# Performance work log

Hardware: AMD Instinct MI355X
Metric: run time of the kernel (lower is better)

The kernel has to match this reference:

```python
import jax, jax.numpy as jnp
import numpy as np

NUM_GRAPHS_N = 64  # number of segments in node_batch
NUM_GRAPHS_L = 64  # number of segments in label_batch


def setup_inputs() -> dict:
    key = jax.random.key(0)
    k1, k2, k3, k4, k5 = jax.random.split(key, 5)
    N, D = 16384, 256
    En, El = 8192, 8192
    h = jax.random.normal(k1, (N, D), dtype=jnp.float32)
    node_edge = jax.random.randint(k2, (2, En), 0, N, dtype=jnp.int64)
    node_batch = jnp.sort(jax.random.randint(k3, (En,), 0, NUM_GRAPHS_N, dtype=jnp.int64))
    label_edge = jax.random.randint(k4, (2, El), 0, N, dtype=jnp.int64)
    label_batch = jnp.sort(jax.random.randint(k5, (El,), 0, NUM_GRAPHS_L, dtype=jnp.int64))
    return {"h": h, "node_edge": node_edge, "node_batch": node_batch,
            "label_edge": label_edge, "label_batch": label_batch}


def _cdist(a, b):
    # Euclidean pairwise distance, grad-safe sqrt.
    sq = (jnp.sum(a * a, -1)[:, None] + jnp.sum(b * b, -1)[None, :]
          - 2.0 * (a @ b.T))
    sq = jnp.maximum(sq, 0.0)
    safe = jnp.where(sq > 0, sq, 1.0)
    return jnp.where(sq > 0, jnp.sqrt(safe), 0.0)


def _seg_max(x, seg, num):  # max over axis 0; empty segments -> 0 like torch_scatter
    m = jax.ops.segment_max(x, seg, num_segments=num)
    return jnp.where(jnp.isfinite(m), m, 0.0)


def _seg_mean(x, seg, num):
    s = jax.ops.segment_sum(x, seg, num_segments=num)
    cnt = jax.ops.segment_sum(jnp.ones((x.shape[0], 1), x.dtype), seg, num_segments=num)
    return s / jnp.maximum(cnt, 1.0)


def reference(h, node_edge, node_batch, label_edge, label_batch):
    ef_n = (h[node_edge[0]] + h[node_edge[1]]) * 0.5   # [En, D]
    ef_l = (h[label_edge[0]] + h[label_edge[1]]) * 0.5  # [El, D]
    M = -_cdist(ef_n, ef_l)                              # [En, El]
    # max over cols by label_batch -> [En, Gl], then mean over rows by node_batch
    out_n = _seg_max(M.T, label_batch, NUM_GRAPHS_L).T   # [En, Gl]
    out_n = _seg_mean(out_n, node_batch, NUM_GRAPHS_N)   # [Gn, Gl]
    # max over rows by node_batch -> [Gn, El], then mean over cols by label_batch
    out_l = _seg_max(M, node_batch, NUM_GRAPHS_N)        # [Gn, El]
    out_l = _seg_mean(out_l.T, label_batch, NUM_GRAPHS_L).T  # [Gn, Gl]
    return (out_n + out_l) * 0.5
```

## Files before the change

### kernel.cpp

```cpp
#include <hip/hip_runtime.h>
#include <hip/hip_bf16.h>
#include <math.h>

#define EN 8192
#define EL 8192
#define D  256
#define NG 64
#define INF_BITS 0x7f800000u

typedef __attribute__((ext_vector_type(8))) short  bf16x8;
typedef __attribute__((ext_vector_type(4))) float  f32x4;

__device__ __forceinline__ unsigned short f2bf(float f) {
    unsigned u = __float_as_uint(f);
    unsigned r = (u + 0x7fffu + ((u >> 16) & 1u)) >> 16;
    return (unsigned short)r;
}

__global__ void prep(const float* __restrict__ h,
                     const int* __restrict__ node_edge,
                     const int* __restrict__ label_edge,
                     unsigned short* __restrict__ efn, float* __restrict__ normN,
                     unsigned short* __restrict__ efl, float* __restrict__ normL,
                     unsigned* __restrict__ inf_buf)
{
    int b = blockIdx.x;
    if (b < 1024) {
        uint4 v = make_uint4(INF_BITS, INF_BITS, INF_BITS, INF_BITS);
        ((uint4*)inf_buf)[b * 256 + threadIdx.x] = v;
        return;
    }
    b -= 1024;
    const int* edges; unsigned short* ef; float* norm;
    if (b < 2048) { edges = node_edge;  ef = efn; norm = normN; }
    else          { b -= 2048; edges = label_edge; ef = efl; norm = normL; }

    int wave = threadIdx.x >> 6;
    int lane = threadIdx.x & 63;
    int e = b * 4 + wave;
    int a  = edges[e];
    int bb = edges[EN + e];
    float4 va = ((const float4*)(h + (size_t)a  * D))[lane];
    float4 vb = ((const float4*)(h + (size_t)bb * D))[lane];
    float4 f;
    f.x = 0.5f * (va.x + vb.x);
    f.y = 0.5f * (va.y + vb.y);
    f.z = 0.5f * (va.z + vb.z);
    f.w = 0.5f * (va.w + vb.w);
    float sq = f.x*f.x + f.y*f.y + f.z*f.z + f.w*f.w;
    ushort4 pk;
    pk.x = f2bf(f.x); pk.y = f2bf(f.y); pk.z = f2bf(f.z); pk.w = f2bf(f.w);
    ((ushort4*)(ef + (size_t)e * D))[lane] = pk;
    #pragma unroll
    for (int off = 1; off < 64; off <<= 1)
        sq += __shfl_xor(sq, off, 64);
    if (lane == 0) norm[e] = sq;
}

__launch_bounds__(512, 4)
__global__ void dist_min(const unsigned short* __restrict__ A,
                         const unsigned short* __restrict__ B,
                         const float* __restrict__ normN,
                         const float* __restrict__ normL,
                         const int* __restrict__ node_batch,
                         const int* __restrict__ label_batch,
                         unsigned* __restrict__ bufN,
                         unsigned* __restrict__ bufL)
{
    __shared__ unsigned short As[128 * 64];
    __shared__ unsigned short Bs[128 * 64];

    const int tid  = threadIdx.x;
    const int lane = tid & 63;
    const int wave = tid >> 6;
    const int quad = lane >> 4;
    const int lc   = lane & 15;
    const int m0   = blockIdx.y * 128;
    const int n0   = blockIdx.x * 128;
    const int wr   = (wave >> 1) * 32;
    const int wc   = (wave & 1) * 64;

    f32x4 acc[2][4];
    #pragma unroll
    for (int i = 0; i < 2; ++i)
        #pragma unroll
        for (int j = 0; j < 4; ++j) {
            f32x4 z = {0.f, 0.f, 0.f, 0.f};
            acc[i][j] = z;
        }

    for (int kt = 0; kt < 4; ++kt) {
        #pragma unroll
        for (int t = 0; t < 2; ++t) {
            int c = t * 512 + tid;
            int row = c >> 3, cc = c & 7;
            int scc = cc ^ (row & 7);
            const unsigned short* gp = A + (size_t)(m0 + row) * D + kt * 64 + scc * 8;
            __builtin_amdgcn_global_load_lds(
                (const __attribute__((address_space(1))) void*)gp,
                (__attribute__((address_space(3))) void*)(As + c * 8), 16, 0, 0);
        }
        #pragma unroll
        for (int t = 0; t < 2; ++t) {
            int c = t * 512 + tid;
            int row = c >> 3, cc = c & 7;
            int scc = cc ^ (row & 7);
            const unsigned short* gp = B + (size_t)(n0 + row) * D + kt * 64 + scc * 8;
            __builtin_amdgcn_global_load_lds(
                (const __attribute__((address_space(1))) void*)gp,
                (__attribute__((address_space(3))) void*)(Bs + c * 8), 16, 0, 0);
        }
        __syncthreads();

        #pragma unroll
        for (int kk = 0; kk < 2; ++kk) {
            bf16x8 af[2], bfv[4];
            #pragma unroll
            for (int mi = 0; mi < 2; ++mi)
                af[mi] = *(const bf16x8*)(As + (wr + mi*16 + lc) * 64
                                             + ((kk*4 + quad) ^ (lc & 7)) * 8);
            #pragma unroll
            for (int ni = 0; ni < 4; ++ni)
                bfv[ni] = *(const bf16x8*)(Bs + (wc + ni*16 + lc) * 64
                                              + ((kk*4 + quad) ^ (lc & 7)) * 8);
            #pragma unroll
            for (int mi = 0; mi < 2; ++mi)
                #pragma unroll
                for (int ni = 0; ni < 4; ++ni)
                    acc[mi][ni] = __builtin_amdgcn_mfma_f32_16x16x32_bf16(
                        af[mi], bfv[ni], acc[mi][ni], 0, 0, 0);
        }
        __syncthreads();
    }

    float nb[4]; int gl[4];
    #pragma unroll
    for (int ni = 0; ni < 4; ++ni) {
        int col = n0 + wc + ni*16 + lc;
        nb[ni] = normL[col];
        gl[ni] = label_batch[col];
    }
    float na[8]; int gr[8];
    #pragma unroll
    for (int mi = 0; mi < 2; ++mi)
        #pragma unroll
        for (int r = 0; r < 4; ++r) {
            int row = m0 + wr + mi*16 + quad*4 + r;
            na[mi*4 + r] = normN[row];
            gr[mi*4 + r] = node_batch[row];
        }

    #pragma unroll
    for (int mi = 0; mi < 2; ++mi)
        #pragma unroll
        for (int ni = 0; ni < 4; ++ni)
            #pragma unroll
            for (int r = 0; r < 4; ++r)
                acc[mi][ni][r] = fmaxf(
                    fmaf(-2.0f, acc[mi][ni][r], na[mi*4 + r] + nb[ni]), 0.0f);

    const float FINF = __uint_as_float(INF_BITS);

    int glo = label_batch[n0 + wc], ghi = label_batch[n0 + wc + 63];
    if (glo == ghi) {
        float rm[8];
        #pragma unroll
        for (int mi = 0; mi < 2; ++mi)
            #pragma unroll
            for (int r = 0; r < 4; ++r) {
                float m = fminf(fminf(acc[mi][0][r], acc[mi][1][r]),
                                fminf(acc[mi][2][r], acc[mi][3][r]));
                m = fminf(m, __shfl_xor(m, 1, 64));
                m = fminf(m, __shfl_xor(m, 2, 64));
                m = fminf(m, __shfl_xor(m, 4, 64));
                m = fminf(m, __shfl_xor(m, 8, 64));
                rm[mi*4 + r] = m;
            }
        if (lc == 0) {
            #pragma unroll
            for (int mi = 0; mi < 2; ++mi)
                #pragma unroll
                for (int r = 0; r < 4; ++r) {
                    int row = m0 + wr + mi*16 + quad*4 + r;
                    atomicMin(&bufN[row * NG + glo], __float_as_uint(rm[mi*4 + r]));
                }
        }
    } else {
        for (int g = glo; g <= ghi; ++g) {
            bool s0 = (gl[0] == g), s1 = (gl[1] == g), s2 = (gl[2] == g), s3 = (gl[3] == g);
            float rm[8];
            #pragma unroll
            for (int mi = 0; mi < 2; ++mi)
                #pragma unroll
                for (int r = 0; r < 4; ++r) {
                    float m = s0 ? acc[mi][0][r] : FINF;
                    m = fminf(m, s1 ? acc[mi][1][r] : FINF);
                    m = fminf(m, s2 ? acc[mi][2][r] : FINF);
                    m = fminf(m, s3 ? acc[mi][3][r] : FINF);
                    m = fminf(m, __shfl_xor(m, 1, 64));
                    m = fminf(m, __shfl_xor(m, 2, 64));
                    m = fminf(m, __shfl_xor(m, 4, 64));
                    m = fminf(m, __shfl_xor(m, 8, 64));
                    rm[mi*4 + r] = m;
                }
            if (lc == 0) {
                #pragma unroll
                for (int mi = 0; mi < 2; ++mi)
                    #pragma unroll
                    for (int r = 0; r < 4; ++r) {
                        int row = m0 + wr + mi*16 + quad*4 + r;
                        atomicMin(&bufN[row * NG + g], __float_as_uint(rm[mi*4 + r]));
                    }
            }
        }
    }

    int rlo = node_batch[m0 + wr], rhi = node_batch[m0 + wr + 31];
    if (rlo == rhi) {
        float cm[4];
        #pragma unroll
        for (int ni = 0; ni < 4; ++ni) {
            float m = acc[0][ni][0];
            m = fminf(m, acc[0][ni][1]); m = fminf(m, acc[0][ni][2]);
            m = fminf(m, acc[0][ni][3]); m = fminf(m, acc[1][ni][0]);
            m = fminf(m, acc[1][ni][1]); m = fminf(m, acc[1][ni][2]);
            m = fminf(m, acc[1][ni][3]);
            m = fminf(m, __shfl_xor(m, 16, 64));
            m = fminf(m, __shfl_xor(m, 32, 64));
            cm[ni] = m;
        }
        if (quad == 0) {
            #pragma unroll
            for (int ni = 0; ni < 4; ++ni) {
                int col = n0 + wc + ni*16 + lc;
                atomicMin(&bufL[rlo * EL + col], __float_as_uint(cm[ni]));
            }
        }
    } else {
        for (int g = rlo; g <= rhi; ++g) {
            float cm[4];
            #pragma unroll
            for (int ni = 0; ni < 4; ++ni) {
                float m = FINF;
                #pragma unroll
                for (int mi = 0; mi < 2; ++mi)
                    #pragma unroll
                    for (int r = 0; r < 4; ++r)
                        m = fminf(m, (gr[mi*4 + r] == g) ? acc[mi][ni][r] : FINF);
                m = fminf(m, __shfl_xor(m, 16, 64));
                m = fminf(m, __shfl_xor(m, 32, 64));
                cm[ni] = m;
            }
            if (quad == 0) {
                #pragma unroll
                for (int ni = 0; ni < 4; ++ni) {
                    int col = n0 + wc + ni*16 + lc;
                    atomicMin(&bufL[g * EL + col], __float_as_uint(cm[ni]));
                }
            }
        }
    }
}

__device__ __forceinline__ int lbound(const int* __restrict__ a, int n, int v) {
    int lo = 0, hi = n;
    while (lo < hi) { int mid = (lo + hi) >> 1; if (a[mid] < v) lo = mid + 1; else hi = mid; }
    return lo;
}

__global__ void finalize(const unsigned* __restrict__ bufN,
                         const unsigned* __restrict__ bufL,
                         const int* __restrict__ node_batch,
                         const int* __restrict__ label_batch,
                         float* __restrict__ out)
{
    __shared__ float sN[NG];
    __shared__ float sL[NG];
    int gn  = blockIdx.x;
    int tid = threadIdx.x;
    if (tid < NG) { sN[tid] = 0.0f; sL[tid] = 0.0f; }
    __syncthreads();

    int ns = lbound(node_batch, EN, gn);
    int ne = lbound(node_batch, EN, gn + 1);

    {
        int t = tid & 63, strip = tid >> 6;
        float acc = 0.0f;
        for (int i = ns + strip; i < ne; i += 16) {
            unsigned b = bufN[i * NG + t];
            if (b != INF_BITS) acc -= sqrtf(__uint_as_float(b));
        }
        atomicAdd(&sN[t], acc);
    }

    for (int j = tid; j < EL; j += 1024) {
        unsigned b = bufL[gn * EL + j];
        if (b != INF_BITS) {
            int g = label_batch[j];
            atomicAdd(&sL[g], -sqrtf(__uint_as_float(b)));
        }
    }
    __syncthreads();

    if (tid < NG) {
        int t = tid;
        int cn = ne - ns;
        int ls = lbound(label_batch, EL, t);
        int le = lbound(label_batch, EL, t + 1);
        int cl = le - ls;
        float out_n = sN[t] / (float)(cn > 0 ? cn : 1);
        float out_l = sL[t] / (float)(cl > 0 ? cl : 1);
        out[gn * NG + t] = 0.5f * (out_n + out_l);
    }
}

extern "C" void kernel_launch(void* const* d_in, const int* in_sizes, int n_in,
                              void* d_out, int out_size, void* d_ws, size_t ws_size,
                              hipStream_t stream)
{
    const float* h          = (const float*)d_in[0];
    const int* node_edge    = (const int*)d_in[1];
    const int* node_batch   = (const int*)d_in[2];
    const int* label_edge   = (const int*)d_in[3];
    const int* label_batch  = (const int*)d_in[4];
    float* out = (float*)d_out;

    char* ws = (char*)d_ws;
    unsigned short* efn = (unsigned short*)ws; ws += (size_t)EN * D * 2;
    unsigned short* efl = (unsigned short*)ws; ws += (size_t)EL * D * 2;
    float* normN = (float*)ws;                 ws += (size_t)EN * 4;
    float* normL = (float*)ws;                 ws += (size_t)EL * 4;
    unsigned* bufN = (unsigned*)ws;            ws += (size_t)EN * NG * 4;
    unsigned* bufL = (unsigned*)ws;            ws += (size_t)NG * EL * 4;

    prep<<<5120, 256, 0, stream>>>(h, node_edge, label_edge,
                                   efn, normN, efl, normL, bufN);
    dist_min<<<dim3(EL / 128, EN / 128), 512, 0, stream>>>(
        efn, efl, normN, normL, node_batch, label_batch, bufN, bufL);
    finalize<<<NG, 1024, 0, stream>>>(bufN, bufL, node_batch, label_batch, out);
}
```

Before: 186.1 us.

## Keep A fragments in registers and double-buffer B tiles in LDS

```diff
diff --git a/kernel.cpp b/kernel.cpp
--- a/kernel.cpp
+++ b/kernel.cpp
@@ -67,8 +67,7 @@
                          unsigned* __restrict__ bufN,
                          unsigned* __restrict__ bufL)
 {
-    __shared__ unsigned short As[128 * 64];
-    __shared__ unsigned short Bs[128 * 64];
+    __shared__ unsigned short Bs[2][128 * 64];
 
     const int tid  = threadIdx.x;
     const int lane = tid & 63;
@@ -80,6 +79,16 @@
     const int wr   = (wave >> 1) * 32;
     const int wc   = (wave & 1) * 64;
 
+    bf16x8 afr[2][8];
+    #pragma unroll
+    for (int mi = 0; mi < 2; ++mi) {
+        const unsigned short* rp =
+            A + (size_t)(m0 + wr + mi*16 + lc) * D + quad*8;
+        #pragma unroll
+        for (int kt = 0; kt < 8; ++kt)
+            afr[mi][kt] = *(const bf16x8*)(rp + kt*32);
+    }
+
     f32x4 acc[2][4];
     #pragma unroll
     for (int i = 0; i < 2; ++i)
@@ -89,48 +98,43 @@
             acc[i][j] = z;
         }
 
-    for (int kt = 0; kt < 4; ++kt) {
+    auto stageB = [&](int kts, int buf) {
         #pragma unroll
         for (int t = 0; t < 2; ++t) {
             int c = t * 512 + tid;
-            int row = c >> 3, cc = c & 7;
-            int scc = cc ^ (row & 7);
-            const unsigned short* gp = A + (size_t)(m0 + row) * D + kt * 64 + scc * 8;
+            int col = c >> 3, cc = c & 7;
+            int scc = cc ^ (col & 7);
+            const unsigned short* gp =
+                B + (size_t)(n0 + col) * D + kts * 64 + scc * 8;
             __builtin_amdgcn_global_load_lds(
                 (const __attribute__((address_space(1))) void*)gp,
-                (__attribute__((address_space(3))) void*)(As + c * 8), 16, 0, 0);
-        }
-        #pragma unroll
-        for (int t = 0; t < 2; ++t) {
-            int c = t * 512 + tid;
-            int row = c >> 3, cc = c & 7;
-            int scc = cc ^ (row & 7);
-            const unsigned short* gp = B + (size_t)(n0 + row) * D + kt * 64 + scc * 8;
-            __builtin_amdgcn_global_load_lds(
-                (const __attribute__((address_space(1))) void*)gp,
-                (__attribute__((address_space(3))) void*)(Bs + c * 8), 16, 0, 0);
-        }
-        __syncthreads();
-
+                (__attribute__((address_space(3))) void*)
+                    (&Bs[buf][col * 64 + cc * 8]), 16, 0, 0);
+        }
+    };
+
+    stageB(0, 0);
+    stageB(1, 1);
+    __syncthreads();
+
+    for (int kts = 0; kts < 4; ++kts) {
+        const int buf = kts & 1;
         #pragma unroll
         for (int kk = 0; kk < 2; ++kk) {
-            bf16x8 af[2], bfv[4];
-            #pragma unroll
-            for (int mi = 0; mi < 2; ++mi)
-                af[mi] = *(const bf16x8*)(As + (wr + mi*16 + lc) * 64
-                                             + ((kk*4 + quad) ^ (lc & 7)) * 8);
+            bf16x8 bfv[4];
             #pragma unroll
             for (int ni = 0; ni < 4; ++ni)
-                bfv[ni] = *(const bf16x8*)(Bs + (wc + ni*16 + lc) * 64
-                                              + ((kk*4 + quad) ^ (lc & 7)) * 8);
+                bfv[ni] = *(const bf16x8*)(&Bs[buf][(wc + ni*16 + lc) * 64
+                                                   + ((kk*4 + quad) ^ (lc & 7)) * 8]);
             #pragma unroll
             for (int mi = 0; mi < 2; ++mi)
                 #pragma unroll
                 for (int ni = 0; ni < 4; ++ni)
                     acc[mi][ni] = __builtin_amdgcn_mfma_f32_16x16x32_bf16(
-                        af[mi], bfv[ni], acc[mi][ni], 0, 0, 0);
+                        afr[mi][kts*2 + kk], bfv[ni], acc[mi][ni], 0, 0, 0);
         }
         __syncthreads();
+        if (kts < 2) stageB(kts + 2, buf);
     }
 
     float nb[4]; int gl[4];
```

New measurement: 219.3 us. +17.8%, slower.

## Make dist_min persistent over column tiles with resident A and double-buffered B

Applied to the files above, without the earlier changes.

```diff
diff --git a/kernel.cpp b/kernel.cpp
--- a/kernel.cpp
+++ b/kernel.cpp
@@ -57,7 +57,7 @@
     if (lane == 0) norm[e] = sq;
 }
 
-__launch_bounds__(512, 4)
+__launch_bounds__(512, 2)
 __global__ void dist_min(const unsigned short* __restrict__ A,
                          const unsigned short* __restrict__ B,
                          const float* __restrict__ normN,
@@ -67,79 +67,50 @@
                          unsigned* __restrict__ bufN,
                          unsigned* __restrict__ bufL)
 {
-    __shared__ unsigned short As[128 * 64];
-    __shared__ unsigned short Bs[128 * 64];
+    __shared__ unsigned short As[128 * 256];
+    __shared__ unsigned short Bs[2][128 * 128];
 
     const int tid  = threadIdx.x;
     const int lane = tid & 63;
     const int wave = tid >> 6;
     const int quad = lane >> 4;
     const int lc   = lane & 15;
-    const int m0   = blockIdx.y * 128;
-    const int n0   = blockIdx.x * 128;
+    const int m0   = (blockIdx.x >> 2) * 128;
+    const int cb   = (blockIdx.x & 3) * 2048;
     const int wr   = (wave >> 1) * 32;
     const int wc   = (wave & 1) * 64;
 
-    f32x4 acc[2][4];
     #pragma unroll
-    for (int i = 0; i < 2; ++i)
+    for (int t = 0; t < 8; ++t) {
+        int c = t * 512 + tid;
+        int row = c >> 5, g = c & 31;
+        const unsigned short* gp =
+            A + (size_t)(m0 + row) * D + (g ^ (row & 7)) * 8;
+        __builtin_amdgcn_global_load_lds(
+            (const __attribute__((address_space(1))) void*)gp,
+            (__attribute__((address_space(3))) void*)(As + row * 256 + g * 8),
+            16, 0, 0);
+    }
+
+    auto stageB = [&](int step) {
+        int ct = step >> 1, s = step & 1;
+        unsigned short* bs = Bs[step & 1];
         #pragma unroll
-        for (int j = 0; j < 4; ++j) {
-            f32x4 z = {0.f, 0.f, 0.f, 0.f};
-            acc[i][j] = z;
-        }
-
-    for (int kt = 0; kt < 4; ++kt) {
-        #pragma unroll
-        for (int t = 0; t < 2; ++t) {
+        for (int t = 0; t < 4; ++t) {
             int c = t * 512 + tid;
-            int row = c >> 3, cc = c & 7;
-            int scc = cc ^ (row & 7);
-            const unsigned short* gp = A + (size_t)(m0 + row) * D + kt * 64 + scc * 8;
+            int col = c >> 4, g = c & 15;
+            const unsigned short* gp =
+                B + (size_t)(cb + ct * 128 + col) * D + s * 128
+                  + (g ^ (col & 7)) * 8;
             __builtin_amdgcn_global_load_lds(
                 (const __attribute__((address_space(1))) void*)gp,
-                (__attribute__((address_space(3))) void*)(As + c * 8), 16, 0, 0);
-        }
-        #pragma unroll
-        for (int t = 0; t < 2; ++t) {
-            int c = t * 512 + tid;
-            int row = c >> 3, cc = c & 7;
-            int scc = cc ^ (row & 7);
-            const unsigned short* gp = B + (size_t)(n0 + row) * D + kt * 64 + scc * 8;
-            __builtin_amdgcn_global_load_lds(
-                (const __attribute__((address_space(1))) void*)gp,
-                (__attribute__((address_space(3))) void*)(Bs + c * 8), 16, 0, 0);
-        }
-        __syncthreads();
-
-        #pragma unroll
-        for (int kk = 0; kk < 2; ++kk) {
-            bf16x8 af[2], bfv[4];
-            #pragma unroll
-            for (int mi = 0; mi < 2; ++mi)
-                af[mi] = *(const bf16x8*)(As + (wr + mi*16 + lc) * 64
-                                             + ((kk*4 + quad) ^ (lc & 7)) * 8);
-            #pragma unroll
-            for (int ni = 0; ni < 4; ++ni)
-                bfv[ni] = *(const bf16x8*)(Bs + (wc + ni*16 + lc) * 64
-                                              + ((kk*4 + quad) ^ (lc & 7)) * 8);
-            #pragma unroll
-            for (int mi = 0; mi < 2; ++mi)
-                #pragma unroll
-                for (int ni = 0; ni < 4; ++ni)
-                    acc[mi][ni] = __builtin_amdgcn_mfma_f32_16x16x32_bf16(
-                        af[mi], bfv[ni], acc[mi][ni], 0, 0, 0);
-        }
-        __syncthreads();
-    }
-
-    float nb[4]; int gl[4];
-    #pragma unroll
-    for (int ni = 0; ni < 4; ++ni) {
-        int col = n0 + wc + ni*16 + lc;
-        nb[ni] = normL[col];
-        gl[ni] = label_batch[col];
-    }
+                (__attribute__((address_space(3))) void*)(bs + col * 128 + g * 8),
+                16, 0, 0);
+        }
+    };
+    stageB(0);
+    stageB(1);
+
     float na[8]; int gr[8];
     #pragma unroll
     for (int mi = 0; mi < 2; ++mi)
@@ -149,115 +120,174 @@
             na[mi*4 + r] = normN[row];
             gr[mi*4 + r] = node_batch[row];
         }
-
+    const int rlo = node_batch[m0 + wr], rhi = node_batch[m0 + wr + 31];
+    const float FINF = __uint_as_float(INF_BITS);
+
+    f32x4 acc[2][4];
     #pragma unroll
-    for (int mi = 0; mi < 2; ++mi)
+    for (int i = 0; i < 2; ++i)
         #pragma unroll
-        for (int ni = 0; ni < 4; ++ni)
-            #pragma unroll
-            for (int r = 0; r < 4; ++r)
-                acc[mi][ni][r] = fmaxf(
-                    fmaf(-2.0f, acc[mi][ni][r], na[mi*4 + r] + nb[ni]), 0.0f);
-
-    const float FINF = __uint_as_float(INF_BITS);
-
-    int glo = label_batch[n0 + wc], ghi = label_batch[n0 + wc + 63];
-    if (glo == ghi) {
-        float rm[8];
+        for (int j = 0; j < 4; ++j) {
+            f32x4 z = {0.f, 0.f, 0.f, 0.f};
+            acc[i][j] = z;
+        }
+
+    __syncthreads();
+
+    for (int step = 0; step < 32; ++step) {
+        const int s = step & 1;
+        const unsigned short* bs = Bs[s];
         #pragma unroll
-        for (int mi = 0; mi < 2; ++mi)
-            #pragma unroll
-            for (int r = 0; r < 4; ++r) {
-                float m = fminf(fminf(acc[mi][0][r], acc[mi][1][r]),
-                                fminf(acc[mi][2][r], acc[mi][3][r]));
-                m = fminf(m, __shfl_xor(m, 1, 64));
-                m = fminf(m, __shfl_xor(m, 2, 64));
-                m = fminf(m, __shfl_xor(m, 4, 64));
-                m = fminf(m, __shfl_xor(m, 8, 64));
-                rm[mi*4 + r] = m;
-            }
-        if (lc == 0) {
+        for (int kk = 0; kk < 4; ++kk) {
+            bf16x8 af[2], bfv[4];
             #pragma unroll
             for (int mi = 0; mi < 2; ++mi)
-                #pragma unroll
-                for (int r = 0; r < 4; ++r) {
-                    int row = m0 + wr + mi*16 + quad*4 + r;
-                    atomicMin(&bufN[row * NG + glo], __float_as_uint(rm[mi*4 + r]));
-                }
-        }
-    } else {
-        for (int g = glo; g <= ghi; ++g) {
-            bool s0 = (gl[0] == g), s1 = (gl[1] == g), s2 = (gl[2] == g), s3 = (gl[3] == g);
-            float rm[8];
+                af[mi] = *(const bf16x8*)(As + (wr + mi*16 + lc) * 256
+                                             + ((s*16 + kk*4 + quad) ^ (lc & 7)) * 8);
+            #pragma unroll
+            for (int ni = 0; ni < 4; ++ni)
+                bfv[ni] = *(const bf16x8*)(bs + (wc + ni*16 + lc) * 128
+                                              + ((kk*4 + quad) ^ (lc & 7)) * 8);
             #pragma unroll
             for (int mi = 0; mi < 2; ++mi)
                 #pragma unroll
-                for (int r = 0; r < 4; ++r) {
-                    float m = s0 ? acc[mi][0][r] : FINF;
-                    m = fminf(m, s1 ? acc[mi][1][r] : FINF);
-                    m = fminf(m, s2 ? acc[mi][2][r] : FINF);
-                    m = fminf(m, s3 ? acc[mi][3][r] : FINF);
-                    m = fminf(m, __shfl_xor(m, 1, 64));
-                    m = fminf(m, __shfl_xor(m, 2, 64));
-                    m = fminf(m, __shfl_xor(m, 4, 64));
-                    m = fminf(m, __shfl_xor(m, 8, 64));
-                    rm[mi*4 + r] = m;
-                }
-            if (lc == 0) {
-                #pragma unroll
-                for (int mi = 0; mi < 2; ++mi)
-                    #pragma unroll
-                    for (int r = 0; r < 4; ++r) {
-                        int row = m0 + wr + mi*16 + quad*4 + r;
-                        atomicMin(&bufN[row * NG + g], __float_as_uint(rm[mi*4 + r]));
-                    }
-            }
-        }
-    }
-
-    int rlo = node_batch[m0 + wr], rhi = node_batch[m0 + wr + 31];
-    if (rlo == rhi) {
-        float cm[4];
-        #pragma unroll
-        for (int ni = 0; ni < 4; ++ni) {
-            float m = acc[0][ni][0];
-            m = fminf(m, acc[0][ni][1]); m = fminf(m, acc[0][ni][2]);
-            m = fminf(m, acc[0][ni][3]); m = fminf(m, acc[1][ni][0]);
-            m = fminf(m, acc[1][ni][1]); m = fminf(m, acc[1][ni][2]);
-            m = fminf(m, acc[1][ni][3]);
-            m = fminf(m, __shfl_xor(m, 16, 64));
-            m = fminf(m, __shfl_xor(m, 32, 64));
-            cm[ni] = m;
-        }
-        if (quad == 0) {
+                for (int ni = 0; ni < 4; ++ni)
+                    acc[mi][ni] = __builtin_amdgcn_mfma_f32_16x16x32_bf16(
+                        af[mi], bfv[ni], acc[mi][ni], 0, 0, 0);
+        }
+        __syncthreads();
+        if (step + 2 < 32) stageB(step + 2);
+
+        if (s == 1) {
+            const int ct = step >> 1;
+            const int n0 = cb + ct * 128;
+
+            float nb[4]; int gl[4];
             #pragma unroll
             for (int ni = 0; ni < 4; ++ni) {
                 int col = n0 + wc + ni*16 + lc;
-                atomicMin(&bufL[rlo * EL + col], __float_as_uint(cm[ni]));
+                nb[ni] = normL[col];
+                gl[ni] = label_batch[col];
             }
-        }
-    } else {
-        for (int g = rlo; g <= rhi; ++g) {
-            float cm[4];
-            #pragma unroll
-            for (int ni = 0; ni < 4; ++ni) {
-                float m = FINF;
+
+            #pragma unroll
+            for (int mi = 0; mi < 2; ++mi)
+                #pragma unroll
+                for (int ni = 0; ni < 4; ++ni)
+                    #pragma unroll
+                    for (int r = 0; r < 4; ++r)
+                        acc[mi][ni][r] = fmaxf(
+                            fmaf(-2.0f, acc[mi][ni][r], na[mi*4 + r] + nb[ni]), 0.0f);
+
+            int glo = label_batch[n0 + wc], ghi = label_batch[n0 + wc + 63];
+            if (glo == ghi) {
+                float rm[8];
                 #pragma unroll
                 for (int mi = 0; mi < 2; ++mi)
                     #pragma unroll
-                    for (int r = 0; r < 4; ++r)
-                        m = fminf(m, (gr[mi*4 + r] == g) ? acc[mi][ni][r] : FINF);
-                m = fminf(m, __shfl_xor(m, 16, 64));
-                m = fminf(m, __shfl_xor(m, 32, 64));
-                cm[ni] = m;
+                    for (int r = 0; r < 4; ++r) {
+                        float m = fminf(fminf(acc[mi][0][r], acc[mi][1][r]),
+                                        fminf(acc[mi][2][r], acc[mi][3][r]));
+                        m = fminf(m, __shfl_xor(m, 1, 64));
+                        m = fminf(m, __shfl_xor(m, 2, 64));
+                        m = fminf(m, __shfl_xor(m, 4, 64));
+                        m = fminf(m, __shfl_xor(m, 8, 64));
+                        rm[mi*4 + r] = m;
+                    }
+                if (lc == 0) {
+                    #pragma unroll
+                    for (int mi = 0; mi < 2; ++mi)
+                        #pragma unroll
+                        for (int r = 0; r < 4; ++r) {
+                            int row = m0 + wr + mi*16 + quad*4 + r;
+                            atomicMin(&bufN[row * NG + glo],
+                                      __float_as_uint(rm[mi*4 + r]));
+                        }
+                }
+            } else {
+                for (int g = glo; g <= ghi; ++g) {
+                    bool s0 = (gl[0] == g), s1 = (gl[1] == g),
+                         s2 = (gl[2] == g), s3 = (gl[3] == g);
+                    float rm[8];
+                    #pragma unroll
+                    for (int mi = 0; mi < 2; ++mi)
+                        #pragma unroll
+                        for (int r = 0; r < 4; ++r) {
+                            float m = s0 ? acc[mi][0][r] : FINF;
+                            m = fminf(m, s1 ? acc[mi][1][r] : FINF);
+                            m = fminf(m, s2 ? acc[mi][2][r] : FINF);
+                            m = fminf(m, s3 ? acc[mi][3][r] : FINF);
+                            m = fminf(m, __shfl_xor(m, 1, 64));
+                            m = fminf(m, __shfl_xor(m, 2, 64));
+                            m = fminf(m, __shfl_xor(m, 4, 64));
+                            m = fminf(m, __shfl_xor(m, 8, 64));
+                            rm[mi*4 + r] = m;
+                        }
+                    if (lc == 0) {
+                        #pragma unroll
+                        for (int mi = 0; mi < 2; ++mi)
+                            #pragma unroll
+                            for (int r = 0; r < 4; ++r) {
+                                int row = m0 + wr + mi*16 + quad*4 + r;
+                                atomicMin(&bufN[row * NG + g],
+                                          __float_as_uint(rm[mi*4 + r]));
+                            }
+                    }
+                }
             }
-            if (quad == 0) {
+
+            if (rlo == rhi) {
+                float cm[4];
                 #pragma unroll
                 for (int ni = 0; ni < 4; ++ni) {
-                    int col = n0 + wc + ni*16 + lc;
-                    atomicMin(&bufL[g * EL + col], __float_as_uint(cm[ni]));
+                    float m = acc[0][ni][0];
+                    m = fminf(m, acc[0][ni][1]); m = fminf(m, acc[0][ni][2]);
+                    m = fminf(m, acc[0][ni][3]); m = fminf(m, acc[1][ni][0]);
+                    m = fminf(m, acc[1][ni][1]); m = fminf(m, acc[1][ni][2]);
+                    m = fminf(m, acc[1][ni][3]);
+                    m = fminf(m, __shfl_xor(m, 16, 64));
+                    m = fminf(m, __shfl_xor(m, 32, 64));
+                    cm[ni] = m;
+                }
+                if (quad == 0) {
+                    #pragma unroll
+                    for (int ni = 0; ni < 4; ++ni) {
+                        int col = n0 + wc + ni*16 + lc;
+                        atomicMin(&bufL[rlo * EL + col], __float_as_uint(cm[ni]));
+                    }
+                }
+            } else {
+                for (int g = rlo; g <= rhi; ++g) {
+                    float cm[4];
+                    #pragma unroll
+                    for (int ni = 0; ni < 4; ++ni) {
+                        float m = FINF;
+                        #pragma unroll
+                        for (int mi = 0; mi < 2; ++mi)
+                            #pragma unroll
+                            for (int r = 0; r < 4; ++r)
+                                m = fminf(m, (gr[mi*4 + r] == g) ? acc[mi][ni][r] : FINF);
+                        m = fminf(m, __shfl_xor(m, 16, 64));
+                        m = fminf(m, __shfl_xor(m, 32, 64));
+                        cm[ni] = m;
+                    }
+                    if (quad == 0) {
+                        #pragma unroll
+                        for (int ni = 0; ni < 4; ++ni) {
+                            int col = n0 + wc + ni*16 + lc;
+                            atomicMin(&bufL[g * EL + col], __float_as_uint(cm[ni]));
+                        }
+                    }
                 }
             }
+
+            #pragma unroll
+            for (int i = 0; i < 2; ++i)
+                #pragma unroll
+                for (int j = 0; j < 4; ++j) {
+                    f32x4 z = {0.f, 0.f, 0.f, 0.f};
+                    acc[i][j] = z;
+                }
         }
     }
 }
@@ -336,7 +366,7 @@
 
     prep<<<5120, 256, 0, stream>>>(h, node_edge, label_edge,
                                    efn, normN, efl, normL, bufN);
-    dist_min<<<dim3(EL / 128, EN / 128), 512, 0, stream>>>(
+    dist_min<<<256, 512, 0, stream>>>(
         efn, efl, normN, normL, node_batch, label_batch, bufN, bufL);
     finalize<<<NG, 1024, 0, stream>>>(bufN, bufL, node_batch, label_batch, out);
 }
```

After: 200.8 us. +7.9%, slower.

## Use 1024-thread blocks with one MFMA row-tile per wave; memset init buffers

Applied to the files above, without the earlier changes.

```diff
diff --git a/kernel.cpp b/kernel.cpp
--- a/kernel.cpp
+++ b/kernel.cpp
@@ -21,16 +21,9 @@
                      const int* __restrict__ node_edge,
                      const int* __restrict__ label_edge,
                      unsigned short* __restrict__ efn, float* __restrict__ normN,
-                     unsigned short* __restrict__ efl, float* __restrict__ normL,
-                     unsigned* __restrict__ inf_buf)
+                     unsigned short* __restrict__ efl, float* __restrict__ normL)
 {
     int b = blockIdx.x;
-    if (b < 1024) {
-        uint4 v = make_uint4(INF_BITS, INF_BITS, INF_BITS, INF_BITS);
-        ((uint4*)inf_buf)[b * 256 + threadIdx.x] = v;
-        return;
-    }
-    b -= 1024;
     const int* edges; unsigned short* ef; float* norm;
     if (b < 2048) { edges = node_edge;  ef = efn; norm = normN; }
     else          { b -= 2048; edges = label_edge; ef = efl; norm = normL; }
@@ -57,7 +50,7 @@
     if (lane == 0) norm[e] = sq;
 }
 
-__launch_bounds__(512, 4)
+__launch_bounds__(1024, 8)
 __global__ void dist_min(const unsigned short* __restrict__ A,
                          const unsigned short* __restrict__ B,
                          const float* __restrict__ normN,
@@ -77,58 +70,44 @@
     const int lc   = lane & 15;
     const int m0   = blockIdx.y * 128;
     const int n0   = blockIdx.x * 128;
-    const int wr   = (wave >> 1) * 32;
+    const int wr   = (wave >> 1) * 16;
     const int wc   = (wave & 1) * 64;
 
-    f32x4 acc[2][4];
-    #pragma unroll
-    for (int i = 0; i < 2; ++i)
-        #pragma unroll
-        for (int j = 0; j < 4; ++j) {
-            f32x4 z = {0.f, 0.f, 0.f, 0.f};
-            acc[i][j] = z;
-        }
+    f32x4 acc[4];
+    #pragma unroll
+    for (int j = 0; j < 4; ++j) {
+        f32x4 z = {0.f, 0.f, 0.f, 0.f};
+        acc[j] = z;
+    }
 
     for (int kt = 0; kt < 4; ++kt) {
-        #pragma unroll
-        for (int t = 0; t < 2; ++t) {
-            int c = t * 512 + tid;
-            int row = c >> 3, cc = c & 7;
+        {
+            int row = tid >> 3, cc = tid & 7;
             int scc = cc ^ (row & 7);
             const unsigned short* gp = A + (size_t)(m0 + row) * D + kt * 64 + scc * 8;
             __builtin_amdgcn_global_load_lds(
                 (const __attribute__((address_space(1))) void*)gp,
-                (__attribute__((address_space(3))) void*)(As + c * 8), 16, 0, 0);
-        }
-        #pragma unroll
-        for (int t = 0; t < 2; ++t) {
-            int c = t * 512 + tid;
-            int row = c >> 3, cc = c & 7;
-            int scc = cc ^ (row & 7);
-            const unsigned short* gp = B + (size_t)(n0 + row) * D + kt * 64 + scc * 8;
+                (__attribute__((address_space(3))) void*)(As + tid * 8), 16, 0, 0);
+            gp = B + (size_t)(n0 + row) * D + kt * 64 + scc * 8;
             __builtin_amdgcn_global_load_lds(
                 (const __attribute__((address_space(1))) void*)gp,
-                (__attribute__((address_space(3))) void*)(Bs + c * 8), 16, 0, 0);
+                (__attribute__((address_space(3))) void*)(Bs + tid * 8), 16, 0, 0);
         }
         __syncthreads();
 
         #pragma unroll
         for (int kk = 0; kk < 2; ++kk) {
-            bf16x8 af[2], bfv[4];
-            #pragma unroll
-            for (int mi = 0; mi < 2; ++mi)
-                af[mi] = *(const bf16x8*)(As + (wr + mi*16 + lc) * 64
-                                             + ((kk*4 + quad) ^ (lc & 7)) * 8);
+            bf16x8 af, bfv[4];
+            af = *(const bf16x8*)(As + (wr + lc) * 64
+                                     + ((kk*4 + quad) ^ (lc & 7)) * 8);
             #pragma unroll
             for (int ni = 0; ni < 4; ++ni)
                 bfv[ni] = *(const bf16x8*)(Bs + (wc + ni*16 + lc) * 64
                                               + ((kk*4 + quad) ^ (lc & 7)) * 8);
             #pragma unroll
-            for (int mi = 0; mi < 2; ++mi)
-                #pragma unroll
-                for (int ni = 0; ni < 4; ++ni)
-                    acc[mi][ni] = __builtin_amdgcn_mfma_f32_16x16x32_bf16(
-                        af[mi], bfv[ni], acc[mi][ni], 0, 0, 0);
+            for (int ni = 0; ni < 4; ++ni)
+                acc[ni] = __builtin_amdgcn_mfma_f32_16x16x32_bf16(
+                    af, bfv[ni], acc[ni], 0, 0, 0);
         }
         __syncthreads();
     }
@@ -140,91 +119,75 @@
         nb[ni] = normL[col];
         gl[ni] = label_batch[col];
     }
-    float na[8]; int gr[8];
-    #pragma unroll
-    for (int mi = 0; mi < 2; ++mi)
+    float na[4]; int gr[4];
+    #pragma unroll
+    for (int r = 0; r < 4; ++r) {
+        int row = m0 + wr + quad*4 + r;
+        na[r] = normN[row];
+        gr[r] = node_batch[row];
+    }
+
+    #pragma unroll
+    for (int ni = 0; ni < 4; ++ni)
+        #pragma unroll
+        for (int r = 0; r < 4; ++r)
+            acc[ni][r] = fmaxf(fmaf(-2.0f, acc[ni][r], na[r] + nb[ni]), 0.0f);
+
+    const float FINF = __uint_as_float(INF_BITS);
+
+    int glo = label_batch[n0 + wc], ghi = label_batch[n0 + wc + 63];
+    if (glo == ghi) {
+        float rm[4];
         #pragma unroll
         for (int r = 0; r < 4; ++r) {
-            int row = m0 + wr + mi*16 + quad*4 + r;
-            na[mi*4 + r] = normN[row];
-            gr[mi*4 + r] = node_batch[row];
-        }
-
-    #pragma unroll
-    for (int mi = 0; mi < 2; ++mi)
-        #pragma unroll
-        for (int ni = 0; ni < 4; ++ni)
-            #pragma unroll
-            for (int r = 0; r < 4; ++r)
-                acc[mi][ni][r] = fmaxf(
-                    fmaf(-2.0f, acc[mi][ni][r], na[mi*4 + r] + nb[ni]), 0.0f);
-
-    const float FINF = __uint_as_float(INF_BITS);
-
-    int glo = label_batch[n0 + wc], ghi = label_batch[n0 + wc + 63];
-    if (glo == ghi) {
-        float rm[8];
-        #pragma unroll
-        for (int mi = 0; mi < 2; ++mi)
+            float m = fminf(fminf(acc[0][r], acc[1][r]),
+                            fminf(acc[2][r], acc[3][r]));
+            m = fminf(m, __shfl_xor(m, 1, 64));
+            m = fminf(m, __shfl_xor(m, 2, 64));
+            m = fminf(m, __shfl_xor(m, 4, 64));
+            m = fminf(m, __shfl_xor(m, 8, 64));
+            rm[r] = m;
+        }
+        if (lc == 0) {
             #pragma unroll
             for (int r = 0; r < 4; ++r) {
-                float m = fminf(fminf(acc[mi][0][r], acc[mi][1][r]),
-                                fminf(acc[mi][2][r], acc[mi][3][r]));
+                int row = m0 + wr + quad*4 + r;
+                atomicMin(&bufN[row * NG + glo], __float_as_uint(rm[r]));
+            }
+        }
+    } else {
+        for (int g = glo; g <= ghi; ++g) {
+            bool s0 = (gl[0] == g), s1 = (gl[1] == g), s2 = (gl[2] == g), s3 = (gl[3] == g);
+            float rm[4];
+            #pragma unroll
+            for (int r = 0; r < 4; ++r) {
+                float m = s0 ? acc[0][r] : FINF;
+                m = fminf(m, s1 ? acc[1][r] : FINF);
+                m = fminf(m, s2 ? acc[2][r] : FINF);
+                m = fminf(m, s3 ? acc[3][r] : FINF);
                 m = fminf(m, __shfl_xor(m, 1, 64));
                 m = fminf(m, __shfl_xor(m, 2, 64));
                 m = fminf(m, __shfl_xor(m, 4, 64));
                 m = fminf(m, __shfl_xor(m, 8, 64));
-                rm[mi*4 + r] = m;
-            }
-        if (lc == 0) {
-            #pragma unroll
-            for (int mi = 0; mi < 2; ++mi)
+                rm[r] = m;
+            }
+            if (lc == 0) {
                 #pragma unroll
                 for (int r = 0; r < 4; ++r) {
-                    int row = m0 + wr + mi*16 + quad*4 + r;
-                    atomicMin(&bufN[row * NG + glo], __float_as_uint(rm[mi*4 + r]));
+                    int row = m0 + wr + quad*4 + r;
+                    atomicMin(&bufN[row * NG + g], __float_as_uint(rm[r]));
                 }
-        }
-    } else {
-        for (int g = glo; g <= ghi; ++g) {
-            bool s0 = (gl[0] == g), s1 = (gl[1] == g), s2 = (gl[2] == g), s3 = (gl[3] == g);
-            float rm[8];
-            #pragma unroll
-            for (int mi = 0; mi < 2; ++mi)
-                #pragma unroll
-                for (int r = 0; r < 4; ++r) {
-                    float m = s0 ? acc[mi][0][r] : FINF;
-                    m = fminf(m, s1 ? acc[mi][1][r] : FINF);
-                    m = fminf(m, s2 ? acc[mi][2][r] : FINF);
-                    m = fminf(m, s3 ? acc[mi][3][r] : FINF);
-                    m = fminf(m, __shfl_xor(m, 1, 64));
-                    m = fminf(m, __shfl_xor(m, 2, 64));
-                    m = fminf(m, __shfl_xor(m, 4, 64));
-                    m = fminf(m, __shfl_xor(m, 8, 64));
-                    rm[mi*4 + r] = m;
-                }
-            if (lc == 0) {
-                #pragma unroll
-                for (int mi = 0; mi < 2; ++mi)
-                    #pragma unroll
-                    for (int r = 0; r < 4; ++r) {
-                        int row = m0 + wr + mi*16 + quad*4 + r;
-                        atomicMin(&bufN[row * NG + g], __float_as_uint(rm[mi*4 + r]));
-                    }
-            }
-        }
-    }
-
-    int rlo = node_batch[m0 + wr], rhi = node_batch[m0 + wr + 31];
+            }
+        }
+    }
+
+    int rlo = node_batch[m0 + wr], rhi = node_batch[m0 + wr + 15];
     if (rlo == rhi) {
         float cm[4];
         #pragma unroll
         for (int ni = 0; ni < 4; ++ni) {
-            float m = acc[0][ni][0];
-            m = fminf(m, acc[0][ni][1]); m = fminf(m, acc[0][ni][2]);
-            m = fminf(m, acc[0][ni][3]); m = fminf(m, acc[1][ni][0]);
-            m = fminf(m, acc[1][ni][1]); m = fminf(m, acc[1][ni][2]);
-            m = fminf(m, acc[1][ni][3]);
+            float m = fminf(fminf(acc[ni][0], acc[ni][1]),
+                            fminf(acc[ni][2], acc[ni][3]));
             m = fminf(m, __shfl_xor(m, 16, 64));
             m = fminf(m, __shfl_xor(m, 32, 64));
             cm[ni] = m;
@@ -243,10 +206,8 @@
             for (int ni = 0; ni < 4; ++ni) {
                 float m = FINF;
                 #pragma unroll
-                for (int mi = 0; mi < 2; ++mi)
-                    #pragma unroll
-                    for (int r = 0; r < 4; ++r)
-                        m = fminf(m, (gr[mi*4 + r] == g) ? acc[mi][ni][r] : FINF);
+                for (int r = 0; r < 4; ++r)
+                    m = fminf(m, (gr[r] == g) ? acc[ni][r] : FINF);
                 m = fminf(m, __shfl_xor(m, 16, 64));
                 m = fminf(m, __shfl_xor(m, 32, 64));
                 cm[ni] = m;
@@ -289,14 +250,14 @@
         float acc = 0.0f;
         for (int i = ns + strip; i < ne; i += 16) {
             unsigned b = bufN[i * NG + t];
-            if (b != INF_BITS) acc -= sqrtf(__uint_as_float(b));
+            if (b < INF_BITS) acc -= sqrtf(__uint_as_float(b));
         }
         atomicAdd(&sN[t], acc);
     }
 
     for (int j = tid; j < EL; j += 1024) {
         unsigned b = bufL[gn * EL + j];
-        if (b != INF_BITS) {
+        if (b < INF_BITS) {
             int g = label_batch[j];
             atomicAdd(&sL[g], -sqrtf(__uint_as_float(b)));
         }
@@ -334,9 +295,10 @@
     unsigned* bufN = (unsigned*)ws;            ws += (size_t)EN * NG * 4;
     unsigned* bufL = (unsigned*)ws;            ws += (size_t)NG * EL * 4;
 
-    prep<<<5120, 256, 0, stream>>>(h, node_edge, label_edge,
-                                   efn, normN, efl, normL, bufN);
-    dist_min<<<dim3(EL / 128, EN / 128), 512, 0, stream>>>(
+    hipMemsetAsync(bufN, 0xFF, (size_t)(EN * NG + NG * EL) * 4, stream);
+    prep<<<4096, 256, 0, stream>>>(h, node_edge, label_edge,
+                                   efn, normN, efl, normL);
+    dist_min<<<dim3(EL / 128, EN / 128), 1024, 0, stream>>>(
         efn, efl, normN, normL, node_batch, label_batch, bufN, bufL);
     finalize<<<NG, 1024, 0, stream>>>(bufN, bufL, node_batch, label_batch, out);
 }
```

Measured after the change: 194.9 us. +4.7%, slower.
